# Kernel tuning notes

Measured on AMD Instinct MI355X. Metric: run time of the kernel, lower is better.

## Reference

```python
import jax, jax.numpy as jnp
from jax import lax
import numpy as np

B, N, D = 64, 1025, 384   # tokens = 1 CLS + 32x32 patch grid
G = 32
K = 8                      # num rotation bases
KS = 8                     # num scale bases
R = 8                      # rank of skew bases
H = 128                    # controller hidden dim
CIN = 3 * D                # cls_mean_var pooling
OUT = D
ROT_GATE_BIAS = -4.0
LOCAL_GATE_BIAS = -3.0


def setup_inputs() -> dict:
    key = jax.random.key(0)
    ks = jax.random.split(key, 16)
    f32 = jnp.float32
    inp = {
        "x": jax.random.normal(ks[0], (B, N, D), f32),
        "shared_weight": jax.random.normal(ks[1], (OUT, D), f32) * 0.02,
        "bias": jnp.zeros((OUT,), f32),
        "left_basis": jax.random.normal(ks[2], (K, D, R), f32) * 0.02,
        "right_basis": jax.random.normal(ks[3], (K, D, R), f32) * 0.02,
        "scale_basis": jax.random.normal(ks[4], (KS, OUT), f32) * 0.01,
        "scale_strength": jnp.asarray(0.25, f32),
        "dw_kernel": jax.random.normal(ks[5], (D, 1, 3, 3), f32) * 0.1,  # depthwise 3x3
        "ctrl_w1": jax.random.normal(ks[6], (H, CIN), f32) * 0.02,
        "ctrl_b1": jnp.zeros((H,), f32),
        "w_rot": jax.random.normal(ks[7], (K, H), f32) * 0.02,
        "b_rot": jnp.zeros((K,), f32),
        "w_rgate": jax.random.normal(ks[8], (1, H), f32) * 0.02,
        "b_rgate": jnp.full((1,), ROT_GATE_BIAS, f32),
        "w_lgate": jax.random.normal(ks[9], (1, H), f32) * 0.02,
        "b_lgate": jnp.full((1,), LOCAL_GATE_BIAS, f32),
        "w_scale": jax.random.normal(ks[10], (KS, H), f32) * 0.02,
        "b_scale": jnp.zeros((KS,), f32),
    }
    return inp


def _forward(x, shared_weight, bias, left_basis, right_basis, scale_basis,
             scale_strength, dw_kernel, ctrl_w1, ctrl_b1, w_rot, b_rot,
             w_rgate, b_rgate, w_lgate, b_lgate, w_scale, b_scale):
    b, n, d = x.shape
    # --- conditioning signal: cls | mean | var (unbiased=False) ---
    cls = x[:, 0]
    mean = jnp.mean(x, axis=1)
    var = jnp.var(x, axis=1)
    z = jnp.concatenate([cls, mean, var], axis=-1)          # [B, 3D]
    # --- controller MLP ---
    h = jax.nn.gelu(z @ ctrl_w1.T + ctrl_b1)                 # [B, H]
    rot_coeff = jnp.tanh(h @ w_rot.T + b_rot)                # [B, K]
    rot_gate = jax.nn.sigmoid(h @ w_rgate.T + b_rgate)[:, 0] # [B]
    local_gate = jax.nn.sigmoid(h @ w_lgate.T + b_lgate)[:, 0]
    scale_coeff = jnp.tanh(h @ w_scale.T + b_scale)          # [B, KS]
    # --- gated local depthwise-conv mixer on the patch grid ---
    cls_tok = x[:, :1, :]
    patch = x[:, 1:, :]                                      # [B, G*G, D]
    grid = patch.transpose(0, 2, 1).reshape(b, d, G, G)      # NCHW
    local = lax.conv_general_dilated(
        grid, dw_kernel, window_strides=(1, 1), padding="SAME",
        feature_group_count=d, dimension_numbers=("NCHW", "OIHW", "NCHW"))
    local_tok = local.reshape(b, d, G * G).transpose(0, 2, 1)
    mixed_patch = patch + local_gate[:, None, None] * (local_tok - patch)
    lm = jnp.concatenate([cls_tok, mixed_patch], axis=1)     # [B, N, D]
    # --- normalized skew bases from low-rank factors ---
    basis = (jnp.einsum("kdr,ker->kde", left_basis, right_basis)
             - jnp.einsum("kdr,ker->kde", right_basis, left_basis))  # [K, D, D]
    norm = jnp.maximum(jnp.linalg.norm(basis.reshape(K, -1), axis=1), 1e-6)
    basis = basis / norm[:, None, None]
    # --- per-sample Cayley rotation (fp32 solve) ---
    skew = jnp.einsum("bk,kde->bde", rot_coeff, basis)       # residual_scale = 1.0
    eye = jnp.eye(d, dtype=jnp.float32)
    half = 0.5 * skew
    transform = jnp.linalg.solve(eye - half, jnp.broadcast_to(eye, half.shape) + half)
    transform = transform.astype(x.dtype)
    # --- gated rotation of features ---
    rotated = jnp.einsum("bnd,bdh->bnh", lm, transform)
    mixed = lm + rot_gate[:, None, None] * (rotated - lm)
    # --- shared linear + dynamic output scaling ---
    preact = mixed @ shared_weight.T + bias                  # [B, N, OUT]
    scale_delta = jnp.tanh(scale_coeff @ scale_basis)        # [B, OUT]
    scale = 1.0 + scale_strength * scale_delta[:, None, :]
    return preact * scale


def reference(x, shared_weight, bias, left_basis, right_basis, scale_basis,
              scale_strength, dw_kernel, ctrl_w1, ctrl_b1, w_rot, b_rot,
              w_rgate, b_rgate, w_lgate, b_lgate, w_scale, b_scale):
    return _forward(x, shared_weight, bias, left_basis, right_basis, scale_basis,
                    scale_strength, dw_kernel, ctrl_w1, ctrl_b1, w_rot, b_rot,
                    w_rgate, b_rgate, w_lgate, b_lgate, w_scale, b_scale)
```

## Files before the change

kernel.cpp:

```cpp
#include <hip/hip_runtime.h>
#include <hip/hip_bf16.h>
#include <math.h>

static const int Bb = 64, Nn = 1025, Dd = 384, Kk = 8, Rr = 8, Hh = 128, CINc = 1152, OUTo = 384;

#define OFF_PSTAT 0u
#define OFF_RC    475136u
#define OFF_RG    475648u
#define OFF_LG    475712u
#define OFF_SCALE 476288u
#define OFF_N2    505472u
#define OFF_P     505600u
#define OFF_Q     554752u
#define OFF_G     603904u
#define OFF_QW    620288u
#define OFF_PB    669440u
#define OFF_EP    694016u
#define OFF_ZT    3839744u
#define OFF_WBT   5412608u
#define OFF_LM    10131200u

typedef __attribute__((ext_vector_type(8))) short short8;
typedef __attribute__((ext_vector_type(8))) __bf16 bf16x8;
typedef __attribute__((ext_vector_type(4))) float f32x4;

#define MFMA_BF16(a,b,c) __builtin_amdgcn_mfma_f32_16x16x32_bf16( \
    __builtin_bit_cast(bf16x8,(a)), __builtin_bit_cast(bf16x8,(b)), (c), 0, 0, 0)

#define GLDS16(gp, lp) __builtin_amdgcn_global_load_lds( \
    (__attribute__((address_space(1))) void*)(gp), \
    (__attribute__((address_space(3))) void*)(lp), 16, 0, 0)

__device__ __forceinline__ float gelu_t(float v){
    float u = 0.7978845608028654f*(v + 0.044715f*v*v*v);
    return 0.5f*v*(1.0f + tanhf(u));
}
__device__ __forceinline__ float sigm(float v){ return 1.0f/(1.0f+expf(-v)); }
__device__ __forceinline__ unsigned short f2bf(float v){
    return __builtin_bit_cast(unsigned short, __float2bfloat16(v));
}

__global__ __launch_bounds__(384) void k_stats(const float* __restrict__ x, float* __restrict__ ps){
    int s = blockIdx.x, b = blockIdx.y, t = threadIdx.x;
    int dq = t % 96, ng = t / 96;
    int n0 = s*129, n1 = n0+129 < Nn ? n0+129 : Nn;
    const float4* xb = (const float4*)(x + (size_t)b*Nn*Dd);
    float4 sm = make_float4(0.f,0.f,0.f,0.f), sq = make_float4(0.f,0.f,0.f,0.f);
    for (int n = n0+ng; n < n1; n += 4){
        float4 v = xb[(size_t)n*96 + dq];
        sm.x += v.x; sm.y += v.y; sm.z += v.z; sm.w += v.w;
        sq.x += v.x*v.x; sq.y += v.y*v.y; sq.z += v.z*v.z; sq.w += v.w*v.w;
    }
    __shared__ float4 smS[384];
    __shared__ float4 sqS[384];
    smS[t] = sm; sqS[t] = sq;
    __syncthreads();
    if (t < 96){
        float4 a0 = smS[t], a1 = smS[t+96], a2 = smS[t+192], a3 = smS[t+288];
        float4 q0 = sqS[t], q1 = sqS[t+96], q2 = sqS[t+192], q3 = sqS[t+288];
        float4 a = make_float4(a0.x+a1.x+a2.x+a3.x, a0.y+a1.y+a2.y+a3.y, a0.z+a1.z+a2.z+a3.z, a0.w+a1.w+a2.w+a3.w);
        float4 q = make_float4(q0.x+q1.x+q2.x+q3.x, q0.y+q1.y+q2.y+q3.y, q0.z+q1.z+q2.z+q3.z, q0.w+q1.w+q2.w+q3.w);
        ((float4*)(ps + ((size_t)(b*8+s)*2+0)*Dd))[t] = a;
        ((float4*)(ps + ((size_t)(b*8+s)*2+1)*Dd))[t] = q;
    }
}

__global__ __launch_bounds__(384) void k_ctrl(const float* __restrict__ x, const float* __restrict__ ps,
    const float* __restrict__ w1, const float* __restrict__ b1,
    const float* __restrict__ w_rot, const float* __restrict__ b_rot,
    const float* __restrict__ w_rg, const float* __restrict__ b_rg,
    const float* __restrict__ w_lg, const float* __restrict__ b_lg,
    const float* __restrict__ w_sc, const float* __restrict__ b_sc,
    const float* __restrict__ sbasis, const float* __restrict__ sstr,
    float* __restrict__ rc, float* __restrict__ rg, float* __restrict__ lg,
    float* __restrict__ scalev, unsigned short* __restrict__ lm){
    __shared__ float zs[1152];
    __shared__ float hp[3*128];
    __shared__ float hs[128];
    __shared__ float scl[8];
    int b = blockIdx.x, t = threadIdx.x;
    float sm = 0.f, sq = 0.f;
    for (int s = 0; s < 8; ++s){
        sm += ps[((size_t)(b*8+s)*2+0)*Dd + t];
        sq += ps[((size_t)(b*8+s)*2+1)*Dd + t];
    }
    float mean = sm*(1.0f/Nn);
    float var  = sq*(1.0f/Nn) - mean*mean;
    float cls  = x[(size_t)b*Nn*Dd + t];
    zs[t] = cls; zs[Dd + t] = mean; zs[2*Dd + t] = var;
    lm[(size_t)b*Nn*Dd + t] = f2bf(cls);
    __syncthreads();
    {
        int row = t & 127, part = t >> 7;
        const float* wrow = w1 + (size_t)row*CINc + part*384;
        const float* zp = zs + part*384;
        float acc = 0.f;
        for (int c = 0; c < 384; ++c) acc += zp[c]*wrow[c];
        hp[part*128 + row] = acc;
    }
    __syncthreads();
    if (t < 128)
        hs[t] = gelu_t(hp[t] + hp[128+t] + hp[256+t] + b1[t]);
    __syncthreads();
    if (t < 8){
        float acc = b_rot[t]; const float* w = w_rot + (size_t)t*Hh;
        for (int c = 0; c < Hh; ++c) acc += hs[c]*w[c];
        rc[b*8+t] = tanhf(acc);
    } else if (t == 8){
        float acc = b_rg[0];
        for (int c = 0; c < Hh; ++c) acc += hs[c]*w_rg[c];
        rg[b] = sigm(acc);
    } else if (t == 9){
        float acc = b_lg[0];
        for (int c = 0; c < Hh; ++c) acc += hs[c]*w_lg[c];
        lg[b] = sigm(acc);
    } else if (t < 18){
        int q = t-10; float acc = b_sc[q]; const float* w = w_sc + (size_t)q*Hh;
        for (int c = 0; c < Hh; ++c) acc += hs[c]*w[c];
        scl[q] = tanhf(acc);
    }
    __syncthreads();
    float acc = 0.f;
    #pragma unroll
    for (int q = 0; q < 8; ++q) acc += scl[q]*sbasis[q*OUTo + t];
    scalev[(size_t)b*OUTo + t] = 1.0f + sstr[0]*tanhf(acc);
}

__global__ __launch_bounds__(256) void k_prep(const float* __restrict__ lb, const float* __restrict__ rb,
                                              float* __restrict__ n2, float* __restrict__ P,
                                              float* __restrict__ Q, unsigned short* __restrict__ Pb){
    int bid = blockIdx.x, t = threadIdx.x;
    if (bid < 8){
        if (t < 64){
            int k = bid;
            int r = t >> 3, s = t & 7;
            const float* L = lb + (size_t)k*Dd*Rr;
            const float* R = rb + (size_t)k*Dd*Rr;
            float a = 0.f, bsum = 0.f, c = 0.f, c2 = 0.f;
            for (int d = 0; d < Dd; ++d){
                float lr = L[d*8+r], ls = L[d*8+s], rr = R[d*8+r], rs = R[d*8+s];
                a += lr*ls; bsum += rr*rs; c += lr*rs; c2 += ls*rr;
            }
            float contrib = a*bsum - c*c2;
            for (int m = 32; m > 0; m >>= 1) contrib += __shfl_xor(contrib, m, 64);
            if (t == 0) n2[k] = 2.f*contrib;
        }
    } else {
        int idx = (bid-8)*256 + t;
        int d = idx >> 7, j = idx & 127;
        int k = (j & 63) >> 3, r = j & 7;
        float lv = lb[((size_t)k*Dd + d)*Rr + r];
        float rv = rb[((size_t)k*Dd + d)*Rr + r];
        float pv = (j < 64) ? lv : rv;
        P[idx] = pv;
        Pb[idx] = f2bf(pv);
        Q[idx] = (j < 64) ? rv : lv;
    }
}

__global__ __launch_bounds__(512) void k_gramqw(const float* __restrict__ P, const float* __restrict__ Q,
                                                const float* __restrict__ Wsh,
                                                float* __restrict__ G, float* __restrict__ QW){
    __shared__ float qc[384];
    int i = blockIdx.x, t = threadIdx.x;
    for (int d = t; d < Dd; d += 512) qc[d] = Q[d*128 + i];
    __syncthreads();
    if (t < 128){
        float a = 0.f;
        for (int d = 0; d < Dd; ++d) a += qc[d]*P[d*128 + t];
        G[i*128 + t] = a;
    } else {
        int o = t - 128;
        float a = 0.f;
        const float* wrow = Wsh + (size_t)o*Dd;
        for (int d = 0; d < Dd; ++d) a += qc[d]*wrow[d];
        QW[(size_t)i*OUTo + o] = a;
    }
}

__global__ __launch_bounds__(512) void k_cayley(const float* __restrict__ G, const float* __restrict__ rc,
                                                const float* __restrict__ n2, const float* __restrict__ rg,
                                                float* __restrict__ Ep){
    __shared__ float GT[128*128];
    __shared__ float Xs[128*128];
    int b = blockIdx.x, t = threadIdx.x;
    for (int lin = t; lin < 16384; lin += 512){
        int i = lin >> 7, m = lin & 127;
        GT[m*128 + i] = G[lin];
    }
    int j0 = (t & 15)*8, i0 = (t >> 4)*4;
    float dj[8], di[4];
    #pragma unroll
    for (int u = 0; u < 8; ++u){
        int j = j0+u; int k = (j&63)>>3;
        float nrm = fmaxf(sqrtf(n2[k]), 1e-6f);
        float al = 0.5f*rc[b*8+k]/nrm;
        dj[u] = (j < 64) ? al : -al;
    }
    #pragma unroll
    for (int u = 0; u < 4; ++u){
        int i = i0+u; int k = (i&63)>>3;
        float nrm = fmaxf(sqrtf(n2[k]), 1e-6f);
        float al = 0.5f*rc[b*8+k]/nrm;
        di[u] = (i < 64) ? al : -al;
    }
    __syncthreads();
    float B0[4][8], acc[4][8];
    #pragma unroll
    for (int ui = 0; ui < 4; ++ui)
        #pragma unroll
        for (int uj = 0; uj < 8; ++uj){
            int i = i0+ui, j = j0+uj;
            float g = GT[j*128 + i];
            B0[ui][uj] = di[ui]*g*dj[uj] + ((i==j) ? di[ui] : 0.f);
        }
    #pragma unroll
    for (int ui = 0; ui < 4; ++ui)
        #pragma unroll
        for (int uj = 0; uj < 8; ++uj)
            Xs[(i0+ui)*128 + j0+uj] = B0[ui][uj];
    __syncthreads();
    for (int pass = 0; pass < 2; ++pass){
        #pragma unroll
        for (int ui = 0; ui < 4; ++ui)
            #pragma unroll
            for (int uj = 0; uj < 8; ++uj) acc[ui][uj] = 0.f;
        for (int m = 0; m < 128; ++m){
            float4 g4 = *(const float4*)&GT[m*128 + i0];
            float4 xa = *(const float4*)&Xs[m*128 + j0];
            float4 xb = *(const float4*)&Xs[m*128 + j0 + 4];
            float gi[4] = {g4.x, g4.y, g4.z, g4.w};
            float xv[8] = {xa.x, xa.y, xa.z, xa.w, xb.x, xb.y, xb.z, xb.w};
            #pragma unroll
            for (int ui = 0; ui < 4; ++ui)
                #pragma unroll
                for (int uj = 0; uj < 8; ++uj)
                    acc[ui][uj] += gi[ui]*xv[uj];
        }
        if (pass == 0){
            __syncthreads();
            #pragma unroll
            for (int ui = 0; ui < 4; ++ui)
                #pragma unroll
                for (int uj = 0; uj < 8; ++uj)
                    Xs[(i0+ui)*128 + j0+uj] = B0[ui][uj] + di[ui]*acc[ui][uj];
            __syncthreads();
        }
    }
    float rgb = rg[b];
    #pragma unroll
    for (int ui = 0; ui < 4; ++ui){
        int i = i0+ui;
        float o[8];
        #pragma unroll
        for (int uj = 0; uj < 8; ++uj){
            int j = j0+uj;
            float x2 = B0[ui][uj] + di[ui]*acc[ui][uj];
            o[uj] = rgb*(x2 + ((i==j) ? di[ui] : 0.f));
        }
        float4* ep4 = (float4*)(Ep + ((size_t)b*128 + i)*128 + j0);
        ep4[0] = make_float4(o[0], o[1], o[2], o[3]);
        ep4[1] = make_float4(o[4], o[5], o[6], o[7]);
    }
}

__global__ __launch_bounds__(384) void k_zmatT(const float* __restrict__ Ep, const float* __restrict__ QW, unsigned short* __restrict__ ZT){
    __shared__ float Es[4*128];
    int ig = blockIdx.x, b = blockIdx.y, t = threadIdx.x;
    int i0 = ig*4;
    for (int lin = t; lin < 512; lin += 384)
        Es[lin] = Ep[((size_t)b*128 + i0 + (lin >> 7))*128 + (lin & 127)];
    __syncthreads();
    float a0=0.f, a1=0.f, a2=0.f, a3=0.f;
    for (int m = 0; m < 128; ++m){
        float qw = QW[(size_t)m*OUTo + t];
        a0 += Es[m]*qw; a1 += Es[128+m]*qw; a2 += Es[256+m]*qw; a3 += Es[384+m]*qw;
    }
    ushort4 uv;
    uv.x = f2bf(a0); uv.y = f2bf(a1); uv.z = f2bf(a2); uv.w = f2bf(a3);
    *(ushort4*)(ZT + ((size_t)b*OUTo + t)*128 + i0) = uv;
}

__global__ __launch_bounds__(256) void k_wbt(const unsigned short* __restrict__ ZT, const unsigned short* __restrict__ Pb,
                                             const float* __restrict__ Wsh, unsigned short* __restrict__ WbT){
    __shared__ short8 As[256];
    __shared__ short8 Bs[256];
    int b = blockIdx.y;
    int mt = blockIdx.x/6, nt2 = blockIdx.x%6;
    int m0 = mt*64, n0 = nt2*64;
    int t = threadIdx.x;
    int w = t>>6, l = t&63;
    int wr = w>>1, wc = w&1;
    const unsigned short* Ab = ZT + (size_t)b*OUTo*128;
    int lrow = t>>2, lseg = t&3;
    f32x4 acc[2][2];
    #pragma unroll
    for (int mi=0;mi<2;++mi)
        #pragma unroll
        for (int ni=0;ni<2;++ni)
            #pragma unroll
            for (int q=0;q<4;++q) acc[mi][ni][q] = 0.f;
    for (int kt = 0; kt < 4; ++kt){
        int k0 = kt*32;
        short8 av = *(const short8*)(Ab + (size_t)(m0+lrow)*128 + k0 + lseg*8);
        short8 bv = *(const short8*)(Pb + (size_t)(n0+lrow)*128 + k0 + lseg*8);
        __syncthreads();
        As[lseg*64 + lrow] = av;
        Bs[lseg*64 + lrow] = bv;
        __syncthreads();
        short8 a0 = As[(l>>4)*64 + wr*32 + (l&15)];
        short8 a1 = As[(l>>4)*64 + wr*32 + 16 + (l&15)];
        short8 b0 = Bs[(l>>4)*64 + wc*32 + (l&15)];
        short8 b1 = Bs[(l>>4)*64 + wc*32 + 16 + (l&15)];
        acc[0][0] = MFMA_BF16(a0, b0, acc[0][0]);
        acc[0][1] = MFMA_BF16(a0, b1, acc[0][1]);
        acc[1][0] = MFMA_BF16(a1, b0, acc[1][0]);
        acc[1][1] = MFMA_BF16(a1, b1, acc[1][1]);
    }
    unsigned short* Wo = WbT + (size_t)b*OUTo*Dd;
    #pragma unroll
    for (int mi=0;mi<2;++mi){
        #pragma unroll
        for (int ni=0;ni<2;++ni){
            int col = n0 + wc*32 + ni*16 + (l&15);
            #pragma unroll
            for (int r=0;r<4;++r){
                int row = m0 + wr*32 + mi*16 + (l>>4)*4 + r;
                float v = Wsh[(size_t)row*Dd + col] + acc[mi][ni][r];
                Wo[(size_t)row*Dd + col] = f2bf(v);
            }
        }
    }
}

__global__ __launch_bounds__(384) void k_lm(const float* __restrict__ x, const float* __restrict__ kw,
                                            const float* __restrict__ lg, unsigned short* __restrict__ lm){
    __shared__ float kws[9*384];
    int flat = blockIdx.x;
    int work = (flat & 7)*256 + (flat >> 3);
    int b = work >> 5, gy = work & 31;
    int t = threadIdx.x;
    for (int i = t; i < 3456; i += 384){
        int d = i % 384, tap = i / 384;
        kws[tap*384 + d] = kw[d*9 + tap];
    }
    __syncthreads();
    int dq = t % 96, gxg = t / 96;
    float lgb = lg[b];
    const float4* xb = (const float4*)(x + (size_t)b*Nn*Dd);
    unsigned short* lmb = lm + (size_t)b*Nn*Dd;
    #pragma unroll
    for (int u = 0; u < 8; ++u){
        int gx = gxg + 4*u;
        int n = 1 + (gy << 5) + gx;
        float4 xc = xb[(size_t)n*96 + dq];
        float ax = 0.f, ay = 0.f, az = 0.f, aw = 0.f;
        #pragma unroll
        for (int ky = 0; ky < 3; ++ky){
            int yy = gy + ky - 1;
            if ((unsigned)yy < 32u){
                #pragma unroll
                for (int kx = 0; kx < 3; ++kx){
                    int xx = gx + kx - 1;
                    if ((unsigned)xx < 32u){
                        float4 xv = xb[(size_t)(1 + (yy << 5) + xx)*96 + dq];
                        const float4 kv = *(const float4*)(&kws[(ky*3+kx)*384 + dq*4]);
                        ax += xv.x*kv.x; ay += xv.y*kv.y; az += xv.z*kv.z; aw += xv.w*kv.w;
                    }
                }
            }
        }
        ushort4 o4;
        o4.x = f2bf(xc.x + lgb*(ax - xc.x));
        o4.y = f2bf(xc.y + lgb*(ay - xc.y));
        o4.z = f2bf(xc.z + lgb*(az - xc.z));
        o4.w = f2bf(xc.w + lgb*(aw - xc.w));
        *(ushort4*)(lmb + (size_t)n*Dd + dq*4) = o4;
    }
}

__global__ __launch_bounds__(256) void k_gemm_nt(const unsigned short* __restrict__ lm, const unsigned short* __restrict__ WbT,
                                                 const float* __restrict__ bias, const float* __restrict__ scalev,
                                                 float* __restrict__ out){
    __shared__ unsigned short smem[16384];
    __shared__ float svs[64];
    __shared__ float bvs[64];
    int flat = blockIdx.x;
    int work = (flat & 7)*816 + (flat >> 3);
    int b = work / 102;
    int r = work - b*102;
    int nt = r / 6, ot = r - nt*6;
    int n0 = nt*64, o0 = ot*64;
    int t = threadIdx.x;
    int w = t >> 6, l = t & 63;
    int wr = w >> 1, wc = w & 1;
    const unsigned short* Ab = lm + (size_t)b*Nn*Dd;
    const unsigned short* Bt = WbT + (size_t)b*OUTo*Dd;
    if (t < 64){ svs[t] = scalev[(size_t)b*OUTo + o0 + t]; bvs[t] = bias[o0 + t]; }
    int srow = l >> 3;
    int sch  = (l & 7) ^ srow;
    f32x4 acc[2][2];
    #pragma unroll
    for (int fi = 0; fi < 2; ++fi)
        #pragma unroll
        for (int fj = 0; fj < 2; ++fj)
            #pragma unroll
            for (int q = 0; q < 4; ++q) acc[fi][fj][q] = 0.f;

#define STAGE(bufi, k0) { \
    unsigned short* Adst = &smem[(bufi)*8192]; \
    unsigned short* Bdst = &smem[(bufi)*8192 + 4096]; \
    _Pragma("unroll") \
    for (int i = 0; i < 2; ++i){ \
        int r0 = (i*4 + w)*8; \
        GLDS16(Ab + (size_t)(n0 + r0 + srow)*Dd + (k0) + sch*8, Adst + r0*64); \
        GLDS16(Bt + (size_t)(o0 + r0 + srow)*Dd + (k0) + sch*8, Bdst + r0*64); \
    } }

    STAGE(0, 0);
    __syncthreads();
    int cur = 0;
    for (int kt = 0; kt < 6; ++kt){
        if (kt < 5) STAGE(cur^1, (kt+1)*64);
        const unsigned short* As  = &smem[cur*8192];
        const unsigned short* Bs2 = &smem[cur*8192 + 4096];
        #pragma unroll
        for (int kc = 0; kc < 2; ++kc){
            short8 a[2], bb[2];
            int ch = (kc*4 + (l>>4)) ^ (l&7);
            #pragma unroll
            for (int f = 0; f < 2; ++f){
                int ra  = wr*32 + f*16 + (l&15);
                int rb2 = wc*32 + f*16 + (l&15);
                a[f]  = *(const short8*)&As [ra*64  + ch*8];
                bb[f] = *(const short8*)&Bs2[rb2*64 + ch*8];
            }
            acc[0][0] = MFMA_BF16(a[0], bb[0], acc[0][0]);
            acc[0][1] = MFMA_BF16(a[0], bb[1], acc[0][1]);
            acc[1][0] = MFMA_BF16(a[1], bb[0], acc[1][0]);
            acc[1][1] = MFMA_BF16(a[1], bb[1], acc[1][1]);
        }
        __syncthreads();
        cur ^= 1;
    }
#undef STAGE
    float* Cs = (float*)smem;
    #pragma unroll
    for (int fi = 0; fi < 2; ++fi)
        #pragma unroll
        for (int fj = 0; fj < 2; ++fj){
            int col = wc*32 + fj*16 + (l&15);
            #pragma unroll
            for (int q = 0; q < 4; ++q){
                int row = wr*32 + fi*16 + (l>>4)*4 + q;
                Cs[row*68 + col] = acc[fi][fj][q];
            }
        }
    __syncthreads();
    #pragma unroll
    for (int p = 0; p < 4; ++p){
        int idx = p*256 + t;
        int row = idx >> 4, c4 = idx & 15;
        int gr = n0 + row;
        if (gr < Nn){
            float4 v = *(const float4*)&Cs[row*68 + c4*4];
            float4 o4;
            o4.x = svs[c4*4+0]*(bvs[c4*4+0] + v.x);
            o4.y = svs[c4*4+1]*(bvs[c4*4+1] + v.y);
            o4.z = svs[c4*4+2]*(bvs[c4*4+2] + v.z);
            o4.w = svs[c4*4+3]*(bvs[c4*4+3] + v.w);
            *(float4*)(out + ((size_t)b*Nn + gr)*OUTo + o0 + c4*4) = o4;
        }
    }
}

extern "C" void kernel_launch(void* const* d_in, const int* in_sizes, int n_in,
                              void* d_out, int out_size, void* d_ws, size_t ws_size,
                              hipStream_t stream){
    const float* x     = (const float*)d_in[0];
    const float* Wsh   = (const float*)d_in[1];
    const float* bias  = (const float*)d_in[2];
    const float* lb    = (const float*)d_in[3];
    const float* rb    = (const float*)d_in[4];
    const float* sbasis= (const float*)d_in[5];
    const float* sstr  = (const float*)d_in[6];
    const float* kw    = (const float*)d_in[7];
    const float* w1    = (const float*)d_in[8];
    const float* b1    = (const float*)d_in[9];
    const float* w_rot = (const float*)d_in[10];
    const float* b_rot = (const float*)d_in[11];
    const float* w_rg  = (const float*)d_in[12];
    const float* b_rg  = (const float*)d_in[13];
    const float* w_lg  = (const float*)d_in[14];
    const float* b_lg  = (const float*)d_in[15];
    const float* w_sc  = (const float*)d_in[16];
    const float* b_sc  = (const float*)d_in[17];
    float* out = (float*)d_out;
    float* ws  = (float*)d_ws;

    float* ps     = ws + OFF_PSTAT;
    float* rc     = ws + OFF_RC;
    float* rg     = ws + OFF_RG;
    float* lg     = ws + OFF_LG;
    float* scalev = ws + OFF_SCALE;
    float* n2     = ws + OFF_N2;
    float* P      = ws + OFF_P;
    float* Q      = ws + OFF_Q;
    float* G      = ws + OFF_G;
    float* QW     = ws + OFF_QW;
    unsigned short* Pb  = (unsigned short*)(ws + OFF_PB);
    float* Ep     = ws + OFF_EP;
    unsigned short* ZT  = (unsigned short*)(ws + OFF_ZT);
    unsigned short* WbT = (unsigned short*)(ws + OFF_WBT);
    unsigned short* lmb = (unsigned short*)(ws + OFF_LM);

    k_stats   <<<dim3(8, Bb), 384, 0, stream>>>(x, ps);
    k_ctrl    <<<Bb, 384, 0, stream>>>(x, ps, w1, b1, w_rot, b_rot, w_rg, b_rg, w_lg, b_lg,
                                       w_sc, b_sc, sbasis, sstr, rc, rg, lg, scalev, lmb);
    k_prep    <<<200, 256, 0, stream>>>(lb, rb, n2, P, Q, Pb);
    k_gramqw  <<<128, 512, 0, stream>>>(P, Q, Wsh, G, QW);
    k_cayley  <<<Bb, 512, 0, stream>>>(G, rc, n2, rg, Ep);
    k_zmatT   <<<dim3(32, Bb), 384, 0, stream>>>(Ep, QW, ZT);
    k_wbt     <<<dim3(36, Bb), 256, 0, stream>>>(ZT, Pb, Wsh, WbT);
    k_lm      <<<2048, 384, 0, stream>>>(x, kw, lg, lmb);
    k_gemm_nt <<<6528, 256, 0, stream>>>(lmb, WbT, bias, scalev, out);
}
```

Measured before the change: 254.6 us.

## Fuse Cayley, Z and weight-build kernels; triple-buffer main GEMM pipeline

The Cayley solve, the Ep×QW product and the low-rank weight update are merged into one per-batch kernel. Intermediates (Ep, ZT) stay in swizzled LDS as bf16, and the Z product now runs on MFMA instead of scalar FMAs. QW is stored transposed in bf16. Separately, the main NT GEMM moves from a 64-wide K step with double buffering to a 32-wide K step with three buffers, using explicit vmcnt waits and raw barriers to keep more loads in flight. The fused kernel runs only 64 blocks and rounds Ep to bf16 earlier, which may cost parallelism and precision.

```diff
diff --git a/kernel.cpp b/kernel.cpp
--- a/kernel.cpp
+++ b/kernel.cpp
@@ -15,8 +15,6 @@
 #define OFF_G     603904u
 #define OFF_QW    620288u
 #define OFF_PB    669440u
-#define OFF_EP    694016u
-#define OFF_ZT    3839744u
 #define OFF_WBT   5412608u
 #define OFF_LM    10131200u
 
@@ -160,7 +158,7 @@
 
 __global__ __launch_bounds__(512) void k_gramqw(const float* __restrict__ P, const float* __restrict__ Q,
                                                 const float* __restrict__ Wsh,
-                                                float* __restrict__ G, float* __restrict__ QW){
+                                                float* __restrict__ G, unsigned short* __restrict__ QWTb){
     __shared__ float qc[384];
     int i = blockIdx.x, t = threadIdx.x;
     for (int d = t; d < Dd; d += 512) qc[d] = Q[d*128 + i];
@@ -174,15 +172,21 @@
         float a = 0.f;
         const float* wrow = Wsh + (size_t)o*Dd;
         for (int d = 0; d < Dd; ++d) a += qc[d]*wrow[d];
-        QW[(size_t)i*OUTo + o] = a;
-    }
-}
-
-__global__ __launch_bounds__(512) void k_cayley(const float* __restrict__ G, const float* __restrict__ rc,
-                                                const float* __restrict__ n2, const float* __restrict__ rg,
-                                                float* __restrict__ Ep){
-    __shared__ float GT[128*128];
-    __shared__ float Xs[128*128];
+        QWTb[(size_t)o*128 + i] = f2bf(a);
+    }
+}
+
+__global__ __launch_bounds__(512) void k_dynw(const float* __restrict__ G, const float* __restrict__ rc,
+                                              const float* __restrict__ n2, const float* __restrict__ rg,
+                                              const unsigned short* __restrict__ QWTb,
+                                              const unsigned short* __restrict__ Pb,
+                                              const float* __restrict__ Wsh,
+                                              unsigned short* __restrict__ WbT){
+    __shared__ float ldsf[32768];
+    float* GT = ldsf;
+    float* Xs = ldsf + 16384;
+    unsigned short* Epb = (unsigned short*)ldsf;
+    unsigned short* ZTl = ((unsigned short*)ldsf) + 16384;
     int b = blockIdx.x, t = threadIdx.x;
     for (int lin = t; lin < 16384; lin += 512){
         int i = lin >> 7, m = lin & 127;
@@ -248,87 +252,58 @@
         }
     }
     float rgb = rg[b];
+    __syncthreads();
     #pragma unroll
     for (int ui = 0; ui < 4; ++ui){
         int i = i0+ui;
-        float o[8];
+        unsigned short o8[8];
         #pragma unroll
         for (int uj = 0; uj < 8; ++uj){
             int j = j0+uj;
             float x2 = B0[ui][uj] + di[ui]*acc[ui][uj];
-            o[uj] = rgb*(x2 + ((i==j) ? di[ui] : 0.f));
-        }
-        float4* ep4 = (float4*)(Ep + ((size_t)b*128 + i)*128 + j0);
-        ep4[0] = make_float4(o[0], o[1], o[2], o[3]);
-        ep4[1] = make_float4(o[4], o[5], o[6], o[7]);
-    }
-}
-
-__global__ __launch_bounds__(384) void k_zmatT(const float* __restrict__ Ep, const float* __restrict__ QW, unsigned short* __restrict__ ZT){
-    __shared__ float Es[4*128];
-    int ig = blockIdx.x, b = blockIdx.y, t = threadIdx.x;
-    int i0 = ig*4;
-    for (int lin = t; lin < 512; lin += 384)
-        Es[lin] = Ep[((size_t)b*128 + i0 + (lin >> 7))*128 + (lin & 127)];
-    __syncthreads();
-    float a0=0.f, a1=0.f, a2=0.f, a3=0.f;
-    for (int m = 0; m < 128; ++m){
-        float qw = QW[(size_t)m*OUTo + t];
-        a0 += Es[m]*qw; a1 += Es[128+m]*qw; a2 += Es[256+m]*qw; a3 += Es[384+m]*qw;
-    }
-    ushort4 uv;
-    uv.x = f2bf(a0); uv.y = f2bf(a1); uv.z = f2bf(a2); uv.w = f2bf(a3);
-    *(ushort4*)(ZT + ((size_t)b*OUTo + t)*128 + i0) = uv;
-}
-
-__global__ __launch_bounds__(256) void k_wbt(const unsigned short* __restrict__ ZT, const unsigned short* __restrict__ Pb,
-                                             const float* __restrict__ Wsh, unsigned short* __restrict__ WbT){
-    __shared__ short8 As[256];
-    __shared__ short8 Bs[256];
-    int b = blockIdx.y;
-    int mt = blockIdx.x/6, nt2 = blockIdx.x%6;
-    int m0 = mt*64, n0 = nt2*64;
-    int t = threadIdx.x;
-    int w = t>>6, l = t&63;
-    int wr = w>>1, wc = w&1;
-    const unsigned short* Ab = ZT + (size_t)b*OUTo*128;
-    int lrow = t>>2, lseg = t&3;
-    f32x4 acc[2][2];
-    #pragma unroll
-    for (int mi=0;mi<2;++mi)
-        #pragma unroll
-        for (int ni=0;ni<2;++ni)
-            #pragma unroll
-            for (int q=0;q<4;++q) acc[mi][ni][q] = 0.f;
-    for (int kt = 0; kt < 4; ++kt){
-        int k0 = kt*32;
-        short8 av = *(const short8*)(Ab + (size_t)(m0+lrow)*128 + k0 + lseg*8);
-        short8 bv = *(const short8*)(Pb + (size_t)(n0+lrow)*128 + k0 + lseg*8);
-        __syncthreads();
-        As[lseg*64 + lrow] = av;
-        Bs[lseg*64 + lrow] = bv;
-        __syncthreads();
-        short8 a0 = As[(l>>4)*64 + wr*32 + (l&15)];
-        short8 a1 = As[(l>>4)*64 + wr*32 + 16 + (l&15)];
-        short8 b0 = Bs[(l>>4)*64 + wc*32 + (l&15)];
-        short8 b1 = Bs[(l>>4)*64 + wc*32 + 16 + (l&15)];
-        acc[0][0] = MFMA_BF16(a0, b0, acc[0][0]);
-        acc[0][1] = MFMA_BF16(a0, b1, acc[0][1]);
-        acc[1][0] = MFMA_BF16(a1, b0, acc[1][0]);
-        acc[1][1] = MFMA_BF16(a1, b1, acc[1][1]);
-    }
+            o8[uj] = f2bf(rgb*(x2 + ((i==j) ? di[ui] : 0.f)));
+        }
+        *(short8*)&Epb[i*128 + (((j0>>3) ^ (i&7))<<3)] = *(short8*)o8;
+    }
+    __syncthreads();
+    int wv = t >> 6, ln = t & 63;
+    for (int ot2 = wv*3; ot2 < wv*3 + 3; ++ot2){
+        for (int it = 0; it < 8; ++it){
+            f32x4 zacc; zacc[0]=0.f; zacc[1]=0.f; zacc[2]=0.f; zacc[3]=0.f;
+            int ii = it*16 + (ln&15);
+            #pragma unroll
+            for (int ks = 0; ks < 4; ++ks){
+                short8 a = *(const short8*)&QWTb[(size_t)(ot2*16 + (ln&15))*128 + ks*32 + (ln>>4)*8];
+                int chb = ((ks*4 + (ln>>4)) ^ (ii&7))*8;
+                short8 bf = *(const short8*)&Epb[ii*128 + chb];
+                zacc = MFMA_BF16(a, bf, zacc);
+            }
+            #pragma unroll
+            for (int rr = 0; rr < 4; ++rr){
+                int o = ot2*16 + (ln>>4)*4 + rr;
+                ZTl[o*128 + (((ii>>3) ^ (o&7))<<3) + (ii&7)] = f2bf(zacc[rr]);
+            }
+        }
+    }
+    __syncthreads();
     unsigned short* Wo = WbT + (size_t)b*OUTo*Dd;
-    #pragma unroll
-    for (int mi=0;mi<2;++mi){
-        #pragma unroll
-        for (int ni=0;ni<2;++ni){
-            int col = n0 + wc*32 + ni*16 + (l&15);
-            #pragma unroll
-            for (int r=0;r<4;++r){
-                int row = m0 + wr*32 + mi*16 + (l>>4)*4 + r;
-                float v = Wsh[(size_t)row*Dd + col] + acc[mi][ni][r];
-                Wo[(size_t)row*Dd + col] = f2bf(v);
-            }
+    for (int tile = wv; tile < 576; tile += 8){
+        int ot2 = tile / 24, dt = tile - (tile/24)*24;
+        f32x4 wacc; wacc[0]=0.f; wacc[1]=0.f; wacc[2]=0.f; wacc[3]=0.f;
+        int oo = ot2*16 + (ln&15);
+        int dd2 = dt*16 + (ln&15);
+        #pragma unroll
+        for (int ks = 0; ks < 4; ++ks){
+            int cha = ((ks*4 + (ln>>4)) ^ (oo&7))*8;
+            short8 a = *(const short8*)&ZTl[oo*128 + cha];
+            short8 bf = *(const short8*)&Pb[(size_t)dd2*128 + ks*32 + (ln>>4)*8];
+            wacc = MFMA_BF16(a, bf, wacc);
+        }
+        #pragma unroll
+        for (int rr = 0; rr < 4; ++rr){
+            int o = ot2*16 + (ln>>4)*4 + rr;
+            int d = dt*16 + (ln&15);
+            Wo[(size_t)o*Dd + d] = f2bf(Wsh[(size_t)o*Dd + d] + wacc[rr]);
         }
     }
 }
@@ -382,7 +357,7 @@
 __global__ __launch_bounds__(256) void k_gemm_nt(const unsigned short* __restrict__ lm, const unsigned short* __restrict__ WbT,
                                                  const float* __restrict__ bias, const float* __restrict__ scalev,
                                                  float* __restrict__ out){
-    __shared__ unsigned short smem[16384];
+    __shared__ unsigned short smem[12288];
     __shared__ float svs[64];
     __shared__ float bvs[64];
     int flat = blockIdx.x;
@@ -397,8 +372,8 @@
     const unsigned short* Ab = lm + (size_t)b*Nn*Dd;
     const unsigned short* Bt = WbT + (size_t)b*OUTo*Dd;
     if (t < 64){ svs[t] = scalev[(size_t)b*OUTo + o0 + t]; bvs[t] = bias[o0 + t]; }
-    int srow = l >> 3;
-    int sch  = (l & 7) ^ srow;
+    int srow = l >> 2;
+    int gch  = (l & 3) ^ ((l >> 3) & 3);
     f32x4 acc[2][2];
     #pragma unroll
     for (int fi = 0; fi < 2; ++fi)
@@ -407,43 +382,38 @@
             #pragma unroll
             for (int q = 0; q < 4; ++q) acc[fi][fj][q] = 0.f;
 
-#define STAGE(bufi, k0) { \
-    unsigned short* Adst = &smem[(bufi)*8192]; \
-    unsigned short* Bdst = &smem[(bufi)*8192 + 4096]; \
-    _Pragma("unroll") \
-    for (int i = 0; i < 2; ++i){ \
-        int r0 = (i*4 + w)*8; \
-        GLDS16(Ab + (size_t)(n0 + r0 + srow)*Dd + (k0) + sch*8, Adst + r0*64); \
-        GLDS16(Bt + (size_t)(o0 + r0 + srow)*Dd + (k0) + sch*8, Bdst + r0*64); \
-    } }
-
-    STAGE(0, 0);
-    __syncthreads();
-    int cur = 0;
-    for (int kt = 0; kt < 6; ++kt){
-        if (kt < 5) STAGE(cur^1, (kt+1)*64);
-        const unsigned short* As  = &smem[cur*8192];
-        const unsigned short* Bs2 = &smem[cur*8192 + 4096];
-        #pragma unroll
-        for (int kc = 0; kc < 2; ++kc){
-            short8 a[2], bb[2];
-            int ch = (kc*4 + (l>>4)) ^ (l&7);
-            #pragma unroll
-            for (int f = 0; f < 2; ++f){
-                int ra  = wr*32 + f*16 + (l&15);
-                int rb2 = wc*32 + f*16 + (l&15);
-                a[f]  = *(const short8*)&As [ra*64  + ch*8];
-                bb[f] = *(const short8*)&Bs2[rb2*64 + ch*8];
-            }
-            acc[0][0] = MFMA_BF16(a[0], bb[0], acc[0][0]);
-            acc[0][1] = MFMA_BF16(a[0], bb[1], acc[0][1]);
-            acc[1][0] = MFMA_BF16(a[1], bb[0], acc[1][0]);
-            acc[1][1] = MFMA_BF16(a[1], bb[1], acc[1][1]);
-        }
-        __syncthreads();
-        cur ^= 1;
-    }
-#undef STAGE
+#define STG(bufi, k0) { \
+    unsigned short* Adst = &smem[(bufi)*4096 + (w*16)*32]; \
+    unsigned short* Bdst = &smem[(bufi)*4096 + 2048 + (w*16)*32]; \
+    GLDS16(Ab + (size_t)(n0 + w*16 + srow)*Dd + (k0) + gch*8, Adst); \
+    GLDS16(Bt + (size_t)(o0 + w*16 + srow)*Dd + (k0) + gch*8, Bdst); }
+
+    STG(0, 0);
+    STG(1, 32);
+    int rch = ((l>>4) ^ (((l&15)>>1)&3)) * 8;
+    int ra0 = (wr*32 + (l&15))*32;
+    int rb0 = (wc*32 + (l&15))*32;
+    for (int kt = 0; kt < 12; ++kt){
+        if (kt < 10) STG((kt+2)%3, (kt+2)*32);
+        if (kt < 10)       asm volatile("s_waitcnt vmcnt(4)" ::: "memory");
+        else if (kt == 10) asm volatile("s_waitcnt vmcnt(2)" ::: "memory");
+        else               asm volatile("s_waitcnt vmcnt(0)" ::: "memory");
+        __builtin_amdgcn_s_barrier();
+        __builtin_amdgcn_sched_barrier(0);
+        const unsigned short* As  = &smem[(kt%3)*4096];
+        const unsigned short* Bs2 = &smem[(kt%3)*4096 + 2048];
+        short8 a0 = *(const short8*)&As [ra0 + rch];
+        short8 a1 = *(const short8*)&As [ra0 + 512 + rch];
+        short8 b0 = *(const short8*)&Bs2[rb0 + rch];
+        short8 b1 = *(const short8*)&Bs2[rb0 + 512 + rch];
+        acc[0][0] = MFMA_BF16(a0, b0, acc[0][0]);
+        acc[0][1] = MFMA_BF16(a0, b1, acc[0][1]);
+        acc[1][0] = MFMA_BF16(a1, b0, acc[1][0]);
+        acc[1][1] = MFMA_BF16(a1, b1, acc[1][1]);
+        __builtin_amdgcn_sched_barrier(0);
+        __builtin_amdgcn_s_barrier();
+    }
+#undef STG
     float* Cs = (float*)smem;
     #pragma unroll
     for (int fi = 0; fi < 2; ++fi)
@@ -507,10 +477,8 @@
     float* P      = ws + OFF_P;
     float* Q      = ws + OFF_Q;
     float* G      = ws + OFF_G;
-    float* QW     = ws + OFF_QW;
+    unsigned short* QWTb = (unsigned short*)(ws + OFF_QW);
     unsigned short* Pb  = (unsigned short*)(ws + OFF_PB);
-    float* Ep     = ws + OFF_EP;
-    unsigned short* ZT  = (unsigned short*)(ws + OFF_ZT);
     unsigned short* WbT = (unsigned short*)(ws + OFF_WBT);
     unsigned short* lmb = (unsigned short*)(ws + OFF_LM);
 
@@ -518,10 +486,8 @@
     k_ctrl    <<<Bb, 384, 0, stream>>>(x, ps, w1, b1, w_rot, b_rot, w_rg, b_rg, w_lg, b_lg,
                                        w_sc, b_sc, sbasis, sstr, rc, rg, lg, scalev, lmb);
     k_prep    <<<200, 256, 0, stream>>>(lb, rb, n2, P, Q, Pb);
-    k_gramqw  <<<128, 512, 0, stream>>>(P, Q, Wsh, G, QW);
-    k_cayley  <<<Bb, 512, 0, stream>>>(G, rc, n2, rg, Ep);
-    k_zmatT   <<<dim3(32, Bb), 384, 0, stream>>>(Ep, QW, ZT);
-    k_wbt     <<<dim3(36, Bb), 256, 0, stream>>>(ZT, Pb, Wsh, WbT);
+    k_gramqw  <<<128, 512, 0, stream>>>(P, Q, Wsh, G, QWTb);
+    k_dynw    <<<Bb, 512, 0, stream>>>(G, rc, n2, rg, QWTb, Pb, Wsh, WbT);
     k_lm      <<<2048, 384, 0, stream>>>(x, kw, lg, lmb);
     k_gemm_nt <<<6528, 256, 0, stream>>>(lmb, WbT, bias, scalev, out);
 }
```

New measurement: 300.8 us. 1.18x slower.
